# Optimization experiments

Measured on AMD Instinct MI355X. Metric: run time of the kernel, lower is better.

Reference implementation:

```python
import jax, jax.numpy as jnp
import numpy as np

NFEAT, NHID, NCLASS = 256, 128, 40
N_NODES, N_EDGES = 50000, 800000
BN_EPS = 1e-5


def setup_inputs() -> dict:
    key = jax.random.key(0)
    ks = jax.random.split(key, 8)
    x = jax.random.normal(ks[0], (N_NODES, NFEAT), dtype=jnp.float32)
    edge_index = jax.random.randint(ks[1], (2, N_EDGES), 0, N_NODES, dtype=jnp.int64)
    # GCNConv layer 0: nfeat -> nhid (Glorot-ish scale)
    W0 = jax.random.normal(ks[2], (NFEAT, NHID), dtype=jnp.float32) / np.sqrt(NFEAT)
    b0 = jnp.zeros((NHID,), dtype=jnp.float32)
    # BatchNorm1d(nhid)
    gamma0 = jnp.ones((NHID,), dtype=jnp.float32)
    beta0 = jnp.zeros((NHID,), dtype=jnp.float32)
    # GCNConv last: nhid -> nclass
    W1 = jax.random.normal(ks[3], (NHID, NCLASS), dtype=jnp.float32) / np.sqrt(NHID)
    b1 = jnp.zeros((NCLASS,), dtype=jnp.float32)
    return {"x": x, "edge_index": edge_index, "W0": W0, "b0": b0,
            "gamma0": gamma0, "beta0": beta0, "W1": W1, "b1": b1}


def _gcn_conv(x, src, dst, W, b, num_nodes):
    # normalize=False GCNConv: linear transform then raw sum aggregation src->dst
    h = x @ W                                   # [N, out]
    out = jax.ops.segment_sum(h[src], dst, num_segments=num_nodes)
    return out + b


def reference(x, edge_index, W0, b0, gamma0, beta0, W1, b1):
    N = x.shape[0]
    src, dst = edge_index[0], edge_index[1]
    # layer 0 conv
    h = _gcn_conv(x, src, dst, W0, b0, N)       # [N, nhid]
    # BatchNorm1d (training-mode batch stats, biased variance)
    mu = h.mean(axis=0)
    var = jnp.mean((h - mu) ** 2, axis=0)
    h = gamma0 * (h - mu) * jax.lax.rsqrt(var + BN_EPS) + beta0
    h = jax.nn.relu(h)
    # (dropout skipped: deterministic eval baseline)
    # last conv (early-return path in original forward)
    out = _gcn_conv(h, src, dst, W1, b1, N)     # [N, nclass]
    return out
```

## Files before the change

### kernel.cpp

```cpp
#include <hip/hip_runtime.h>
#include <hip/hip_fp8.h>

#define NFEAT 256
#define NHID 128
#define NCLASS 40
#define NNODES 50000
#define NEDGES 800000
#define BN_EPS 1e-5f
#define NBK 196
#define NBLK 100
#define EPB 8000
#define NW1H 3125
#define G1H_BLOCKS 782

typedef __attribute__((ext_vector_type(4))) float f32x4;
typedef __attribute__((ext_vector_type(8))) short bf16x8;

__device__ inline ushort f2bf(float f) {
    uint u = __float_as_uint(f);
    u += 0x7FFF + ((u >> 16) & 1);
    return (ushort)(u >> 16);
}
__device__ inline float bflo(uint v) { return __uint_as_float(v << 16); }
__device__ inline float bfhi(uint v) { return __uint_as_float(v & 0xFFFF0000u); }

__device__ inline uint pk_fp8x4(float a0, float a1, float a2, float a3) {
#if __has_builtin(__builtin_amdgcn_cvt_pk_fp8_f32)
    int u = 0;
    u = __builtin_amdgcn_cvt_pk_fp8_f32(a0, a1, u, false);
    u = __builtin_amdgcn_cvt_pk_fp8_f32(a2, a3, u, true);
    return (uint)u;
#else
    __hip_fp8_e4m3 q0(a0), q1(a1), q2(a2), q3(a3);
    return (uint)q0.__x | ((uint)q1.__x << 8) | ((uint)q2.__x << 16) | ((uint)q3.__x << 24);
#endif
}
__device__ inline float fp8lo(uint v) {
#if __has_builtin(__builtin_amdgcn_cvt_f32_fp8)
    return __builtin_amdgcn_cvt_f32_fp8((int)v, 0);
#else
    __hip_fp8_e4m3 q; q.__x = (__hip_fp8_storage_t)(v & 0xFF); return (float)q;
#endif
}
__device__ inline float fp8hi(uint v) {
#if __has_builtin(__builtin_amdgcn_cvt_f32_fp8)
    return __builtin_amdgcn_cvt_f32_fp8((int)v, 1);
#else
    __hip_fp8_e4m3 q; q.__x = (__hip_fp8_storage_t)((v >> 8) & 0xFF); return (float)q;
#endif
}

__device__ inline void gemm1_half(int gt, int half, const float* __restrict__ x,
                                  const ushort* __restrict__ W0F, uchar* __restrict__ h1) {
    const int w = gt >> 6;
    if (w >= NW1H) return;
    const int lane = gt & 63;
    const int node = w * 16 + (lane & 15);
    const int nclamp = node < NNODES ? node : NNODES - 1;
    const float* xg = &x[(long)nclamp * NFEAT + (lane >> 4) * 8];

    float4 xa[8], xb[8];
    #pragma unroll
    for (int kc = 0; kc < 8; ++kc) {
        xa[kc] = *(const float4*)(xg + kc * 32);
        xb[kc] = *(const float4*)(xg + kc * 32 + 4);
    }
    __builtin_amdgcn_sched_barrier(0);
    bf16x8 xf[8];
    #pragma unroll
    for (int kc = 0; kc < 8; ++kc) {
        xf[kc][0]=(short)f2bf(xa[kc].x); xf[kc][1]=(short)f2bf(xa[kc].y);
        xf[kc][2]=(short)f2bf(xa[kc].z); xf[kc][3]=(short)f2bf(xa[kc].w);
        xf[kc][4]=(short)f2bf(xb[kc].x); xf[kc][5]=(short)f2bf(xb[kc].y);
        xf[kc][6]=(short)f2bf(xb[kc].z); xf[kc][7]=(short)f2bf(xb[kc].w);
    }
    __builtin_amdgcn_sched_barrier(0);
    f32x4 acc[4];
    #pragma unroll
    for (int f = 0; f < 4; ++f) acc[f] = (f32x4){0.f, 0.f, 0.f, 0.f};
    const ushort* wbase = &W0F[(size_t)(gt & 63) * 8];
    #pragma unroll
    for (int kc = 0; kc < 8; ++kc) {
        #pragma unroll
        for (int f = 0; f < 4; ++f) {
            const int grp = (half * 4 + f) * 8 + kc;
            const bf16x8 wf = *(const bf16x8*)&wbase[(size_t)grp * 64 * 8];
            acc[f] = __builtin_amdgcn_mfma_f32_16x16x32_bf16(wf, xf[kc], acc[f], 0, 0, 0);
        }
    }
    if (node < NNODES) {
        const int nq = (lane >> 4) * 4;
        uchar* hp = &h1[(long)node * NHID + half * 64 + nq];
        #pragma unroll
        for (int f = 0; f < 4; ++f)
            *(uint*)&hp[f * 16] = pk_fp8x4(acc[f][0], acc[f][1], acc[f][2], acc[f][3]);
    }
}

__global__ void k_prep(const float* __restrict__ W0, ushort* __restrict__ W0F,
                       const int* __restrict__ ei, int* __restrict__ bcnt,
                       float* __restrict__ stats, int* __restrict__ rowptr) {
    __shared__ int cnt[NBK];
    if (blockIdx.x < 16) {
        if (blockIdx.x == 0) {
            stats[threadIdx.x] = 0.f;
            if (threadIdx.x == 0) rowptr[NNODES] = NEDGES;
        }
        const int t = blockIdx.x * 256 + threadIdx.x;
        const int lane = t & 63;
        const int grp = t >> 6;
        const int kc = grp & 7, fi = grp >> 3;
        const int n = fi * 16 + (lane & 15);
        const int k0 = kc * 32 + (lane >> 4) * 8;
        ushort v[8];
        #pragma unroll
        for (int j = 0; j < 8; ++j) v[j] = f2bf(W0[(k0 + j) * NHID + n]);
        uint4 u;
        u.x = (uint)v[0] | ((uint)v[1] << 16);
        u.y = (uint)v[2] | ((uint)v[3] << 16);
        u.z = (uint)v[4] | ((uint)v[5] << 16);
        u.w = (uint)v[6] | ((uint)v[7] << 16);
        *(uint4*)&W0F[(grp * 64 + lane) * 8] = u;
    } else {
        const int blk = blockIdx.x - 16;
        const int t = threadIdx.x;
        if (t < NBK) cnt[t] = 0;
        __syncthreads();
        const int base = blk * EPB;
        for (int i = t; i < EPB; i += 256)
            atomicAdd(&cnt[ei[NEDGES + base + i] >> 8], 1);
        __syncthreads();
        if (t < NBK) bcnt[blk * NBK + t] = cnt[t];
    }
}

__launch_bounds__(256, 1)
__global__ void k_scatter_g1(const int* __restrict__ ei, const int* __restrict__ bcnt,
                             uint* __restrict__ packed,
                             const float* __restrict__ x, const ushort* __restrict__ W0F,
                             uchar* __restrict__ h1) {
    __shared__ int s_sc[256], s_cur[256];
    if (blockIdx.x < NBLK) {
        const int tid = threadIdx.x, blk = blockIdx.x;
        int tot = 0, pre = 0;
        if (tid < NBK) {
            for (int bb = 0; bb < NBLK; ++bb) {
                const int v = bcnt[bb * NBK + tid];
                tot += v;
                if (bb < blk) pre += v;
            }
        }
        s_sc[tid] = tot;
        __syncthreads();
        for (int o = 1; o < 256; o <<= 1) {
            const int v = (tid >= o) ? s_sc[tid - o] : 0;
            __syncthreads();
            s_sc[tid] += v;
            __syncthreads();
        }
        s_cur[tid] = (s_sc[tid] - tot) + pre;
        __syncthreads();
        const int base = blk * EPB;
        for (int i = tid; i < EPB; i += 256) {
            const int src = ei[base + i];
            const int dst = ei[NEDGES + base + i];
            const int pos = atomicAdd(&s_cur[dst >> 8], 1);
            packed[pos] = (uint)src | ((uint)(dst & 255) << 16);
        }
    } else {
        gemm1_half((blockIdx.x - NBLK) * 256 + threadIdx.x, 0, x, W0F, h1);
    }
}

__launch_bounds__(256, 1)
__global__ void k_sort_g1(const uint* __restrict__ packed, const int* __restrict__ bcnt,
                          int* __restrict__ esrc, int* __restrict__ rowptr,
                          const float* __restrict__ x, const ushort* __restrict__ W0F,
                          uchar* __restrict__ h1) {
    __shared__ int s_cnt[256], s_sc[256], s_cur[256];
    __shared__ int s_seg[2];
    if (blockIdx.x < NBK) {
        const int b = blockIdx.x, tid = threadIdx.x;
        int tot = 0;
        if (tid < NBK)
            for (int bb = 0; bb < NBLK; ++bb) tot += bcnt[bb * NBK + tid];
        s_sc[tid] = tot;
        __syncthreads();
        for (int o = 1; o < 256; o <<= 1) {
            const int v = (tid >= o) ? s_sc[tid - o] : 0;
            __syncthreads();
            s_sc[tid] += v;
            __syncthreads();
        }
        if (tid == b) { s_seg[0] = s_sc[b] - tot; s_seg[1] = s_sc[b]; }
        __syncthreads();
        const int nb = s_seg[0], ne = s_seg[1], n = ne - nb;
        s_cnt[tid] = 0;
        __syncthreads();
        for (int i = tid; i < n; i += 256)
            atomicAdd(&s_cnt[packed[nb + i] >> 16], 1);
        __syncthreads();
        const int v = s_cnt[tid];
        s_sc[tid] = v;
        __syncthreads();
        for (int o = 1; o < 256; o <<= 1) {
            const int tmp = (tid >= o) ? s_sc[tid - o] : 0;
            __syncthreads();
            s_sc[tid] += tmp;
            __syncthreads();
        }
        const int excl = s_sc[tid] - v;
        s_cur[tid] = excl;
        const int node = (b << 8) + tid;
        if (node < NNODES) rowptr[node] = nb + excl;
        __syncthreads();
        for (int i = tid; i < n; i += 256) {
            const uint p = packed[nb + i];
            const int pos = atomicAdd(&s_cur[p >> 16], 1);
            esrc[nb + pos] = (int)(p & 0xFFFFu);
        }
    } else {
        gemm1_half((blockIdx.x - NBK) * 256 + threadIdx.x, 1, x, W0F, h1);
    }
}

__launch_bounds__(256)
__global__ void k_gather1(const int* __restrict__ rowptr, const int* __restrict__ esrc,
                          const uchar* __restrict__ h1, const float* __restrict__ b0,
                          float* __restrict__ agg1) {
    const int w = (blockIdx.x * blockDim.x + threadIdx.x) >> 6;
    const int lane = threadIdx.x & 63;
    if (w >= NNODES) return;
    const int beg = rowptr[w], end = rowptr[w + 1];
    const int f = lane * 2;
    float2 acc = *(const float2*)&b0[f];
    int i = beg;
    for (; i + 7 < end; i += 8) {
        uint v[8];
        #pragma unroll
        for (int j = 0; j < 8; ++j)
            v[j] = (uint)*(const ushort*)&h1[(long)esrc[i + j] * NHID + f];
        #pragma unroll
        for (int j = 0; j < 8; ++j) { acc.x += fp8lo(v[j]); acc.y += fp8hi(v[j]); }
    }
    for (; i < end; ++i) {
        const uint v = (uint)*(const ushort*)&h1[(long)esrc[i] * NHID + f];
        acc.x += fp8lo(v); acc.y += fp8hi(v);
    }
    *(float2*)&agg1[(long)w * NHID + f] = acc;
}

__global__ void k_bnstats(const float* __restrict__ agg1,
                          float* __restrict__ sums, float* __restrict__ sumsq) {
    __shared__ float sd[256 * 4], sd2[256 * 4];
    const int t = threadIdx.x;
    const int c4 = (t & 31) * 4;
    const int rr = t >> 5;
    float4 s = make_float4(0.f,0.f,0.f,0.f), s2 = s;
    for (int r = blockIdx.x * 8 + rr; r < NNODES; r += gridDim.x * 8) {
        const float4 v = *(const float4*)&agg1[(long)r * NHID + c4];
        s.x += v.x; s.y += v.y; s.z += v.z; s.w += v.w;
        s2.x += v.x*v.x; s2.y += v.y*v.y; s2.z += v.z*v.z; s2.w += v.w*v.w;
    }
    *(float4*)&sd[t * 4] = s; *(float4*)&sd2[t * 4] = s2;
    __syncthreads();
    if (t < 32) {
        #pragma unroll
        for (int j = 1; j < 8; ++j) {
            const float4 a = *(const float4*)&sd[(j * 32 + t) * 4];
            const float4 a2 = *(const float4*)&sd2[(j * 32 + t) * 4];
            s = *(float4*)&sd[t * 4];
            s2 = *(float4*)&sd2[t * 4];
            s.x += a.x; s.y += a.y; s.z += a.z; s.w += a.w;
            s2.x += a2.x; s2.y += a2.y; s2.z += a2.z; s2.w += a2.w;
            *(float4*)&sd[t * 4] = s; *(float4*)&sd2[t * 4] = s2;
        }
        atomicAdd(&sums[c4 + 0], s.x);  atomicAdd(&sums[c4 + 1], s.y);
        atomicAdd(&sums[c4 + 2], s.z);  atomicAdd(&sums[c4 + 3], s.w);
        atomicAdd(&sumsq[c4 + 0], s2.x); atomicAdd(&sumsq[c4 + 1], s2.y);
        atomicAdd(&sumsq[c4 + 2], s2.z); atomicAdd(&sumsq[c4 + 3], s2.w);
    }
}

__launch_bounds__(256)
__global__ void k_gemm2(const float* __restrict__ agg1, const float* __restrict__ W1,
                        const float* __restrict__ sums, const float* __restrict__ sumsq,
                        const float* __restrict__ gamma, const float* __restrict__ beta,
                        ushort* __restrict__ h2) {
    __shared__ float xs[64 * 132];
    __shared__ float wt[40 * 132];
    __shared__ float s_scale[128], s_shift[128];
    const int t = threadIdx.x;
    const int base = blockIdx.x * 64;

    if (t < NHID) {
        const float mu = sums[t] * (1.f / NNODES);
        float var = sumsq[t] * (1.f / NNODES) - mu * mu;
        var = fmaxf(var, 0.f);
        const float sc = gamma[t] * rsqrtf(var + BN_EPS);
        s_scale[t] = sc;
        s_shift[t] = beta[t] - mu * sc;
    }
    for (int idx = t; idx < NHID * NCLASS; idx += 256) {
        const int c = idx / NCLASS, j = idx % NCLASS;
        wt[j * 132 + c] = W1[idx];
    }
    __syncthreads();
    {
        const int cc = (t & 31) * 4;
        const float4 sc = *(const float4*)&s_scale[cc];
        const float4 sh = *(const float4*)&s_shift[cc];
        const int rb = t >> 5;
        #pragma unroll
        for (int p = 0; p < 8; ++p) {
            const int row = p * 8 + rb;
            const int g = base + row;
            float4 v = make_float4(0.f, 0.f, 0.f, 0.f);
            if (g < NNODES) {
                const float4 a = *(const float4*)&agg1[(long)g * NHID + cc];
                v.x = fmaxf(a.x * sc.x + sh.x, 0.f);
                v.y = fmaxf(a.y * sc.y + sh.y, 0.f);
                v.z = fmaxf(a.z * sc.z + sh.z, 0.f);
                v.w = fmaxf(a.w * sc.w + sh.w, 0.f);
            }
            *(float4*)&xs[row * 132 + cc] = v;
        }
    }
    __syncthreads();

    const int node = t >> 2;
    const int j0 = (t & 3) * 10;
    float acc[10] = {};
    for (int c4 = 0; c4 < 32; ++c4) {
        const int c = c4 * 4;
        const float4 a = *(const float4*)&xs[node * 132 + c];
        #pragma unroll
        for (int jj = 0; jj < 10; ++jj) {
            const float4 wv = *(const float4*)&wt[(j0 + jj) * 132 + c];
            acc[jj] += a.x * wv.x + a.y * wv.y + a.z * wv.z + a.w * wv.w;
        }
    }
    const int g = base + node;
    if (g < NNODES) {
        #pragma unroll
        for (int p = 0; p < 5; ++p) {
            uint u = (uint)f2bf(acc[2 * p]) | ((uint)f2bf(acc[2 * p + 1]) << 16);
            *(uint*)&h2[(long)g * NCLASS + j0 + 2 * p] = u;
        }
    }
}

__launch_bounds__(256)
__global__ void k_gather2(const int* __restrict__ rowptr, const int* __restrict__ esrc,
                          const ushort* __restrict__ h2, const float* __restrict__ b1,
                          float* __restrict__ out) {
    const int t = threadIdx.x;
    if (t >= 240) return;
    const int node = blockIdx.x * 12 + t / 20;
    if (node >= NNODES) return;
    const int f = (t % 20) * 2;
    const int beg = rowptr[node], end = rowptr[node + 1];
    float2 acc = make_float2(b1[f], b1[f + 1]);
    int i = beg;
    for (; i + 3 < end; i += 4) {
        const uint v0 = *(const uint*)&h2[(long)esrc[i]     * NCLASS + f];
        const uint v1 = *(const uint*)&h2[(long)esrc[i + 1] * NCLASS + f];
        const uint v2 = *(const uint*)&h2[(long)esrc[i + 2] * NCLASS + f];
        const uint v3 = *(const uint*)&h2[(long)esrc[i + 3] * NCLASS + f];
        acc.x += (bflo(v0) + bflo(v1)) + (bflo(v2) + bflo(v3));
        acc.y += (bfhi(v0) + bfhi(v1)) + (bfhi(v2) + bfhi(v3));
    }
    for (; i < end; ++i) {
        const uint v = *(const uint*)&h2[(long)esrc[i] * NCLASS + f];
        acc.x += bflo(v); acc.y += bfhi(v);
    }
    *(float2*)&out[(long)node * NCLASS + f] = acc;
}

extern "C" void kernel_launch(void* const* d_in, const int* in_sizes, int n_in,
                              void* d_out, int out_size, void* d_ws, size_t ws_size,
                              hipStream_t stream) {
    const float* x      = (const float*)d_in[0];
    const int*   ei     = (const int*)d_in[1];
    const float* W0     = (const float*)d_in[2];
    const float* b0     = (const float*)d_in[3];
    const float* gamma0 = (const float*)d_in[4];
    const float* beta0  = (const float*)d_in[5];
    const float* W1     = (const float*)d_in[6];
    const float* b1     = (const float*)d_in[7];
    float* out = (float*)d_out;

    char* ws = (char*)d_ws;
    float* sums  = (float*)ws;
    float* sumsq = sums + 128;
    int* wsI     = (int*)(ws + 4096);
    int* rowptr  = wsI;
    int* esrc    = wsI + 50048;
    int* bcnt    = wsI + 850048;
    ushort* W0F  = (ushort*)(ws + 3563520);
    uchar* h1    = (uchar*)(ws + 3629056);
    float* agg1  = (float*)(ws + 16429056);
    uint* packed = (uint*)agg1;
    ushort* h2   = (ushort*)h1;

    k_prep<<<16 + NBLK, 256, 0, stream>>>(W0, W0F, ei, bcnt, sums, rowptr);
    k_scatter_g1<<<NBLK + G1H_BLOCKS, 256, 0, stream>>>(ei, bcnt, packed, x, W0F, h1);
    k_sort_g1<<<NBK + G1H_BLOCKS, 256, 0, stream>>>(packed, bcnt, esrc, rowptr, x, W0F, h1);
    k_gather1<<<(NNODES * 64 + 255) / 256, 256, 0, stream>>>(rowptr, esrc, h1, b0, agg1);
    k_bnstats<<<256, 256, 0, stream>>>(agg1, sums, sumsq);
    k_gemm2<<<(NNODES + 63) / 64, 256, 0, stream>>>(agg1, W1, sums, sumsq, gamma0, beta0, h2);
    k_gather2<<<(NNODES + 11) / 12, 256, 0, stream>>>(rowptr, esrc, h2, b1, out);
}
```

Measured before the change: 173.1 us.

## Fuse BN statistics into gather1, store agg1 as bf16, move whole gemm1 to scatter

```diff
diff --git a/kernel.cpp b/kernel.cpp
--- a/kernel.cpp
+++ b/kernel.cpp
@@ -10,8 +10,10 @@
 #define NBK 196
 #define NBLK 100
 #define EPB 8000
-#define NW1H 3125
-#define G1H_BLOCKS 782
+#define BKCAP 6144
+#define NW1 6250
+#define GEMM1_BLOCKS 1563
+#define G1_BLOCKS 2048
 
 typedef __attribute__((ext_vector_type(4))) float f32x4;
 typedef __attribute__((ext_vector_type(8))) short bf16x8;
@@ -48,53 +50,6 @@
 #else
     __hip_fp8_e4m3 q; q.__x = (__hip_fp8_storage_t)((v >> 8) & 0xFF); return (float)q;
 #endif
-}
-
-__device__ inline void gemm1_half(int gt, int half, const float* __restrict__ x,
-                                  const ushort* __restrict__ W0F, uchar* __restrict__ h1) {
-    const int w = gt >> 6;
-    if (w >= NW1H) return;
-    const int lane = gt & 63;
-    const int node = w * 16 + (lane & 15);
-    const int nclamp = node < NNODES ? node : NNODES - 1;
-    const float* xg = &x[(long)nclamp * NFEAT + (lane >> 4) * 8];
-
-    float4 xa[8], xb[8];
-    #pragma unroll
-    for (int kc = 0; kc < 8; ++kc) {
-        xa[kc] = *(const float4*)(xg + kc * 32);
-        xb[kc] = *(const float4*)(xg + kc * 32 + 4);
-    }
-    __builtin_amdgcn_sched_barrier(0);
-    bf16x8 xf[8];
-    #pragma unroll
-    for (int kc = 0; kc < 8; ++kc) {
-        xf[kc][0]=(short)f2bf(xa[kc].x); xf[kc][1]=(short)f2bf(xa[kc].y);
-        xf[kc][2]=(short)f2bf(xa[kc].z); xf[kc][3]=(short)f2bf(xa[kc].w);
-        xf[kc][4]=(short)f2bf(xb[kc].x); xf[kc][5]=(short)f2bf(xb[kc].y);
-        xf[kc][6]=(short)f2bf(xb[kc].z); xf[kc][7]=(short)f2bf(xb[kc].w);
-    }
-    __builtin_amdgcn_sched_barrier(0);
-    f32x4 acc[4];
-    #pragma unroll
-    for (int f = 0; f < 4; ++f) acc[f] = (f32x4){0.f, 0.f, 0.f, 0.f};
-    const ushort* wbase = &W0F[(size_t)(gt & 63) * 8];
-    #pragma unroll
-    for (int kc = 0; kc < 8; ++kc) {
-        #pragma unroll
-        for (int f = 0; f < 4; ++f) {
-            const int grp = (half * 4 + f) * 8 + kc;
-            const bf16x8 wf = *(const bf16x8*)&wbase[(size_t)grp * 64 * 8];
-            acc[f] = __builtin_amdgcn_mfma_f32_16x16x32_bf16(wf, xf[kc], acc[f], 0, 0, 0);
-        }
-    }
-    if (node < NNODES) {
-        const int nq = (lane >> 4) * 4;
-        uchar* hp = &h1[(long)node * NHID + half * 64 + nq];
-        #pragma unroll
-        for (int f = 0; f < 4; ++f)
-            *(uint*)&hp[f * 16] = pk_fp8x4(acc[f][0], acc[f][1], acc[f][2], acc[f][3]);
-    }
 }
 
 __global__ void k_prep(const float* __restrict__ W0, ushort* __restrict__ W0F,
@@ -135,10 +90,10 @@
 }
 
 __launch_bounds__(256, 1)
-__global__ void k_scatter_g1(const int* __restrict__ ei, const int* __restrict__ bcnt,
-                             uint* __restrict__ packed,
-                             const float* __restrict__ x, const ushort* __restrict__ W0F,
-                             uchar* __restrict__ h1) {
+__global__ void k_scatter_gemm1(const int* __restrict__ ei, const int* __restrict__ bcnt,
+                                uint* __restrict__ packed,
+                                const float* __restrict__ x, const ushort* __restrict__ W0F,
+                                uchar* __restrict__ h1) {
     __shared__ int s_sc[256], s_cur[256];
     if (blockIdx.x < NBLK) {
         const int tid = threadIdx.x, blk = blockIdx.x;
@@ -168,122 +123,146 @@
             packed[pos] = (uint)src | ((uint)(dst & 255) << 16);
         }
     } else {
-        gemm1_half((blockIdx.x - NBLK) * 256 + threadIdx.x, 0, x, W0F, h1);
-    }
-}
-
-__launch_bounds__(256, 1)
-__global__ void k_sort_g1(const uint* __restrict__ packed, const int* __restrict__ bcnt,
-                          int* __restrict__ esrc, int* __restrict__ rowptr,
-                          const float* __restrict__ x, const ushort* __restrict__ W0F,
-                          uchar* __restrict__ h1) {
+        const int gt = (blockIdx.x - NBLK) * 256 + threadIdx.x;
+        const int w = gt >> 6;
+        if (w >= NW1) return;
+        const int lane = gt & 63;
+        const int half = w & 1;
+        const int node = (w >> 1) * 16 + (lane & 15);
+        const int nclamp = node < NNODES ? node : NNODES - 1;
+        const float* xg = &x[(long)nclamp * NFEAT + (lane >> 4) * 8];
+
+        float4 xa[8], xb[8];
+        #pragma unroll
+        for (int kc = 0; kc < 8; ++kc) {
+            xa[kc] = *(const float4*)(xg + kc * 32);
+            xb[kc] = *(const float4*)(xg + kc * 32 + 4);
+        }
+        __builtin_amdgcn_sched_barrier(0);
+        bf16x8 xf[8];
+        #pragma unroll
+        for (int kc = 0; kc < 8; ++kc) {
+            xf[kc][0]=(short)f2bf(xa[kc].x); xf[kc][1]=(short)f2bf(xa[kc].y);
+            xf[kc][2]=(short)f2bf(xa[kc].z); xf[kc][3]=(short)f2bf(xa[kc].w);
+            xf[kc][4]=(short)f2bf(xb[kc].x); xf[kc][5]=(short)f2bf(xb[kc].y);
+            xf[kc][6]=(short)f2bf(xb[kc].z); xf[kc][7]=(short)f2bf(xb[kc].w);
+        }
+        __builtin_amdgcn_sched_barrier(0);
+        f32x4 acc[4];
+        #pragma unroll
+        for (int f = 0; f < 4; ++f) acc[f] = (f32x4){0.f, 0.f, 0.f, 0.f};
+        const ushort* wbase = &W0F[(size_t)lane * 8];
+        #pragma unroll
+        for (int kc = 0; kc < 8; ++kc) {
+            #pragma unroll
+            for (int f = 0; f < 4; ++f) {
+                const int grp = (half * 4 + f) * 8 + kc;
+                const bf16x8 wf = *(const bf16x8*)&wbase[(size_t)grp * 64 * 8];
+                acc[f] = __builtin_amdgcn_mfma_f32_16x16x32_bf16(wf, xf[kc], acc[f], 0, 0, 0);
+            }
+        }
+        if (node < NNODES) {
+            const int nq = (lane >> 4) * 4;
+            uchar* hp = &h1[(long)node * NHID + half * 64 + nq];
+            #pragma unroll
+            for (int f = 0; f < 4; ++f)
+                *(uint*)&hp[f * 16] = pk_fp8x4(acc[f][0], acc[f][1], acc[f][2], acc[f][3]);
+        }
+    }
+}
+
+__launch_bounds__(256)
+__global__ void k_bksort(const uint* __restrict__ packed, const int* __restrict__ bcnt,
+                         int* __restrict__ esrc, int* __restrict__ rowptr) {
     __shared__ int s_cnt[256], s_sc[256], s_cur[256];
     __shared__ int s_seg[2];
-    if (blockIdx.x < NBK) {
-        const int b = blockIdx.x, tid = threadIdx.x;
-        int tot = 0;
-        if (tid < NBK)
-            for (int bb = 0; bb < NBLK; ++bb) tot += bcnt[bb * NBK + tid];
-        s_sc[tid] = tot;
-        __syncthreads();
-        for (int o = 1; o < 256; o <<= 1) {
-            const int v = (tid >= o) ? s_sc[tid - o] : 0;
-            __syncthreads();
-            s_sc[tid] += v;
-            __syncthreads();
-        }
-        if (tid == b) { s_seg[0] = s_sc[b] - tot; s_seg[1] = s_sc[b]; }
-        __syncthreads();
-        const int nb = s_seg[0], ne = s_seg[1], n = ne - nb;
-        s_cnt[tid] = 0;
-        __syncthreads();
-        for (int i = tid; i < n; i += 256)
-            atomicAdd(&s_cnt[packed[nb + i] >> 16], 1);
-        __syncthreads();
-        const int v = s_cnt[tid];
-        s_sc[tid] = v;
-        __syncthreads();
-        for (int o = 1; o < 256; o <<= 1) {
-            const int tmp = (tid >= o) ? s_sc[tid - o] : 0;
-            __syncthreads();
-            s_sc[tid] += tmp;
-            __syncthreads();
-        }
-        const int excl = s_sc[tid] - v;
-        s_cur[tid] = excl;
-        const int node = (b << 8) + tid;
-        if (node < NNODES) rowptr[node] = nb + excl;
-        __syncthreads();
-        for (int i = tid; i < n; i += 256) {
-            const uint p = packed[nb + i];
-            const int pos = atomicAdd(&s_cur[p >> 16], 1);
-            esrc[nb + pos] = (int)(p & 0xFFFFu);
-        }
-    } else {
-        gemm1_half((blockIdx.x - NBK) * 256 + threadIdx.x, 1, x, W0F, h1);
+    const int b = blockIdx.x, tid = threadIdx.x;
+    int tot = 0;
+    if (tid < NBK)
+        for (int bb = 0; bb < NBLK; ++bb) tot += bcnt[bb * NBK + tid];
+    s_sc[tid] = tot;
+    __syncthreads();
+    for (int o = 1; o < 256; o <<= 1) {
+        const int v = (tid >= o) ? s_sc[tid - o] : 0;
+        __syncthreads();
+        s_sc[tid] += v;
+        __syncthreads();
+    }
+    if (tid == b) { s_seg[0] = s_sc[b] - tot; s_seg[1] = s_sc[b]; }
+    __syncthreads();
+    const int nb = s_seg[0], ne = s_seg[1], n = ne - nb;
+    s_cnt[tid] = 0;
+    __syncthreads();
+    for (int i = tid; i < n; i += 256)
+        atomicAdd(&s_cnt[packed[nb + i] >> 16], 1);
+    __syncthreads();
+    const int v = s_cnt[tid];
+    s_sc[tid] = v;
+    __syncthreads();
+    for (int o = 1; o < 256; o <<= 1) {
+        const int tmp = (tid >= o) ? s_sc[tid - o] : 0;
+        __syncthreads();
+        s_sc[tid] += tmp;
+        __syncthreads();
+    }
+    const int excl = s_sc[tid] - v;
+    s_cur[tid] = excl;
+    const int node = (b << 8) + tid;
+    if (node < NNODES) rowptr[node] = nb + excl;
+    __syncthreads();
+    for (int i = tid; i < n; i += 256) {
+        const uint p = packed[nb + i];
+        const int pos = atomicAdd(&s_cur[p >> 16], 1);
+        esrc[nb + pos] = (int)(p & 0xFFFFu);
     }
 }
 
 __launch_bounds__(256)
 __global__ void k_gather1(const int* __restrict__ rowptr, const int* __restrict__ esrc,
                           const uchar* __restrict__ h1, const float* __restrict__ b0,
-                          float* __restrict__ agg1) {
-    const int w = (blockIdx.x * blockDim.x + threadIdx.x) >> 6;
-    const int lane = threadIdx.x & 63;
-    if (w >= NNODES) return;
-    const int beg = rowptr[w], end = rowptr[w + 1];
+                          ushort* __restrict__ agg1bf,
+                          float* __restrict__ sums, float* __restrict__ sumsq) {
+    __shared__ float s_bns[4][128], s_bnq[4][128];
+    const int wv = threadIdx.x >> 6, lane = threadIdx.x & 63;
     const int f = lane * 2;
-    float2 acc = *(const float2*)&b0[f];
-    int i = beg;
-    for (; i + 7 < end; i += 8) {
-        uint v[8];
-        #pragma unroll
-        for (int j = 0; j < 8; ++j)
-            v[j] = (uint)*(const ushort*)&h1[(long)esrc[i + j] * NHID + f];
-        #pragma unroll
-        for (int j = 0; j < 8; ++j) { acc.x += fp8lo(v[j]); acc.y += fp8hi(v[j]); }
-    }
-    for (; i < end; ++i) {
-        const uint v = (uint)*(const ushort*)&h1[(long)esrc[i] * NHID + f];
-        acc.x += fp8lo(v); acc.y += fp8hi(v);
-    }
-    *(float2*)&agg1[(long)w * NHID + f] = acc;
-}
-
-__global__ void k_bnstats(const float* __restrict__ agg1,
-                          float* __restrict__ sums, float* __restrict__ sumsq) {
-    __shared__ float sd[256 * 4], sd2[256 * 4];
-    const int t = threadIdx.x;
-    const int c4 = (t & 31) * 4;
-    const int rr = t >> 5;
-    float4 s = make_float4(0.f,0.f,0.f,0.f), s2 = s;
-    for (int r = blockIdx.x * 8 + rr; r < NNODES; r += gridDim.x * 8) {
-        const float4 v = *(const float4*)&agg1[(long)r * NHID + c4];
-        s.x += v.x; s.y += v.y; s.z += v.z; s.w += v.w;
-        s2.x += v.x*v.x; s2.y += v.y*v.y; s2.z += v.z*v.z; s2.w += v.w*v.w;
-    }
-    *(float4*)&sd[t * 4] = s; *(float4*)&sd2[t * 4] = s2;
-    __syncthreads();
-    if (t < 32) {
-        #pragma unroll
-        for (int j = 1; j < 8; ++j) {
-            const float4 a = *(const float4*)&sd[(j * 32 + t) * 4];
-            const float4 a2 = *(const float4*)&sd2[(j * 32 + t) * 4];
-            s = *(float4*)&sd[t * 4];
-            s2 = *(float4*)&sd2[t * 4];
-            s.x += a.x; s.y += a.y; s.z += a.z; s.w += a.w;
-            s2.x += a2.x; s2.y += a2.y; s2.z += a2.z; s2.w += a2.w;
-            *(float4*)&sd[t * 4] = s; *(float4*)&sd2[t * 4] = s2;
-        }
-        atomicAdd(&sums[c4 + 0], s.x);  atomicAdd(&sums[c4 + 1], s.y);
-        atomicAdd(&sums[c4 + 2], s.z);  atomicAdd(&sums[c4 + 3], s.w);
-        atomicAdd(&sumsq[c4 + 0], s2.x); atomicAdd(&sumsq[c4 + 1], s2.y);
-        atomicAdd(&sumsq[c4 + 2], s2.z); atomicAdd(&sumsq[c4 + 3], s2.w);
+    const float2 bias = *(const float2*)&b0[f];
+    float2 bns = make_float2(0.f, 0.f), bnq = make_float2(0.f, 0.f);
+
+    for (int w = blockIdx.x * 4 + wv; w < NNODES; w += G1_BLOCKS * 4) {
+        const int beg = rowptr[w], end = rowptr[w + 1];
+        float2 acc = bias;
+        int i = beg;
+        for (; i + 7 < end; i += 8) {
+            uint v[8];
+            #pragma unroll
+            for (int j = 0; j < 8; ++j)
+                v[j] = (uint)*(const ushort*)&h1[(long)esrc[i + j] * NHID + f];
+            #pragma unroll
+            for (int j = 0; j < 8; ++j) { acc.x += fp8lo(v[j]); acc.y += fp8hi(v[j]); }
+        }
+        for (; i < end; ++i) {
+            const uint v = (uint)*(const ushort*)&h1[(long)esrc[i] * NHID + f];
+            acc.x += fp8lo(v); acc.y += fp8hi(v);
+        }
+        const uint u = (uint)f2bf(acc.x) | ((uint)f2bf(acc.y) << 16);
+        *(uint*)&agg1bf[(long)w * NHID + f] = u;
+        bns.x += acc.x; bns.y += acc.y;
+        bnq.x += acc.x * acc.x; bnq.y += acc.y * acc.y;
+    }
+    s_bns[wv][f] = bns.x; s_bns[wv][f + 1] = bns.y;
+    s_bnq[wv][f] = bnq.x; s_bnq[wv][f + 1] = bnq.y;
+    __syncthreads();
+    if (threadIdx.x < 128) {
+        const int c = threadIdx.x;
+        const float s = (s_bns[0][c] + s_bns[1][c]) + (s_bns[2][c] + s_bns[3][c]);
+        const float q = (s_bnq[0][c] + s_bnq[1][c]) + (s_bnq[2][c] + s_bnq[3][c]);
+        atomicAdd(&sums[c], s);
+        atomicAdd(&sumsq[c], q);
     }
 }
 
 __launch_bounds__(256)
-__global__ void k_gemm2(const float* __restrict__ agg1, const float* __restrict__ W1,
+__global__ void k_gemm2(const ushort* __restrict__ agg1bf, const float* __restrict__ W1,
                         const float* __restrict__ sums, const float* __restrict__ sumsq,
                         const float* __restrict__ gamma, const float* __restrict__ beta,
                         ushort* __restrict__ h2) {
@@ -307,23 +286,22 @@
     }
     __syncthreads();
     {
-        const int cc = (t & 31) * 4;
-        const float4 sc = *(const float4*)&s_scale[cc];
-        const float4 sh = *(const float4*)&s_shift[cc];
-        const int rb = t >> 5;
-        #pragma unroll
-        for (int p = 0; p < 8; ++p) {
-            const int row = p * 8 + rb;
+        const int cc = (t & 15) * 8;
+        const int rb = t >> 4;
+        #pragma unroll
+        for (int p = 0; p < 4; ++p) {
+            const int row = p * 16 + rb;
             const int g = base + row;
-            float4 v = make_float4(0.f, 0.f, 0.f, 0.f);
-            if (g < NNODES) {
-                const float4 a = *(const float4*)&agg1[(long)g * NHID + cc];
-                v.x = fmaxf(a.x * sc.x + sh.x, 0.f);
-                v.y = fmaxf(a.y * sc.y + sh.y, 0.f);
-                v.z = fmaxf(a.z * sc.z + sh.z, 0.f);
-                v.w = fmaxf(a.w * sc.w + sh.w, 0.f);
+            uint4 u = make_uint4(0u, 0u, 0u, 0u);
+            if (g < NNODES) u = *(const uint4*)&agg1bf[(long)g * NHID + cc];
+            const uint uu[4] = {u.x, u.y, u.z, u.w};
+            #pragma unroll
+            for (int q = 0; q < 4; ++q) {
+                const int c0 = cc + q * 2;
+                const float a0 = bflo(uu[q]), a1 = bfhi(uu[q]);
+                xs[row * 132 + c0]     = fmaxf(a0 * s_scale[c0]     + s_shift[c0],     0.f);
+                xs[row * 132 + c0 + 1] = fmaxf(a1 * s_scale[c0 + 1] + s_shift[c0 + 1], 0.f);
             }
-            *(float4*)&xs[row * 132 + cc] = v;
         }
     }
     __syncthreads();
@@ -399,15 +377,14 @@
     int* bcnt    = wsI + 850048;
     ushort* W0F  = (ushort*)(ws + 3563520);
     uchar* h1    = (uchar*)(ws + 3629056);
-    float* agg1  = (float*)(ws + 16429056);
-    uint* packed = (uint*)agg1;
+    ushort* agg1bf = (ushort*)(ws + 16429056);
+    uint* packed = (uint*)agg1bf;
     ushort* h2   = (ushort*)h1;
 
     k_prep<<<16 + NBLK, 256, 0, stream>>>(W0, W0F, ei, bcnt, sums, rowptr);
-    k_scatter_g1<<<NBLK + G1H_BLOCKS, 256, 0, stream>>>(ei, bcnt, packed, x, W0F, h1);
-    k_sort_g1<<<NBK + G1H_BLOCKS, 256, 0, stream>>>(packed, bcnt, esrc, rowptr, x, W0F, h1);
-    k_gather1<<<(NNODES * 64 + 255) / 256, 256, 0, stream>>>(rowptr, esrc, h1, b0, agg1);
-    k_bnstats<<<256, 256, 0, stream>>>(agg1, sums, sumsq);
-    k_gemm2<<<(NNODES + 63) / 64, 256, 0, stream>>>(agg1, W1, sums, sumsq, gamma0, beta0, h2);
+    k_scatter_gemm1<<<NBLK + GEMM1_BLOCKS, 256, 0, stream>>>(ei, bcnt, packed, x, W0F, h1);
+    k_bksort<<<NBK, 256, 0, stream>>>(packed, bcnt, esrc, rowptr);
+    k_gather1<<<G1_BLOCKS, 256, 0, stream>>>(rowptr, esrc, h1, b0, agg1bf, sums, sumsq);
+    k_gemm2<<<(NNODES + 63) / 64, 256, 0, stream>>>(agg1bf, W1, sums, sumsq, gamma0, beta0, h2);
     k_gather2<<<(NNODES + 11) / 12, 256, 0, stream>>>(rowptr, esrc, h2, b1, out);
 }
```

Result: slower. 179.1 us (+3.5%).
